# Performance work log

Measured on AMD Instinct MI355X. Metric: run time of the kernel, lower is better.

## Reference

```python
import jax, jax.numpy as jnp
import numpy as np

N_SRC, N_DST, E = 32768, 8192, 65536
NODE_IN, EDGE_IN, HIDDEN = 64, 32, 64


def setup_inputs() -> dict:
    key = jax.random.key(0)
    ks = jax.random.split(key, 8)
    node_features = jax.random.normal(ks[0], (N_SRC, NODE_IN), dtype=jnp.float32)
    edge_features = jax.random.normal(ks[1], (E, EDGE_IN), dtype=jnp.float32)
    src_idx = jax.random.randint(ks[2], (E,), 0, N_SRC, dtype=jnp.int32)
    dst_idx = jax.random.randint(ks[3], (E,), 0, N_DST, dtype=jnp.int32)
    # edge_layer: Linear(edge_in, hidden*node_in); node_layer: Linear(node_in+hidden, hidden)
    s_e = 1.0 / np.sqrt(EDGE_IN)
    s_n = 1.0 / np.sqrt(NODE_IN + HIDDEN)
    W_e = jax.random.uniform(ks[4], (EDGE_IN, HIDDEN * NODE_IN), jnp.float32, -s_e, s_e)
    b_e = jax.random.uniform(ks[5], (HIDDEN * NODE_IN,), jnp.float32, -s_e, s_e)
    W_n = jax.random.uniform(ks[6], (NODE_IN + HIDDEN, HIDDEN), jnp.float32, -s_n, s_n)
    b_n = jax.random.uniform(ks[7], (HIDDEN,), jnp.float32, -s_n, s_n)
    return {"node_features": node_features, "edge_features": edge_features,
            "src_idx": src_idx, "dst_idx": dst_idx,
            "W_e": W_e, "b_e": b_e, "W_n": W_n, "b_n": b_n, "n_dst": N_DST}


def reference(node_features, edge_features, src_idx, dst_idx, W_e, b_e, W_n, b_n, n_dst):
    # Dropout is identity in eval mode.
    # Edge-conditioned weight generation: [E, hidden*node_in] -> [E, hidden, node_in]
    ew = jax.nn.relu(edge_features @ W_e + b_e).reshape(-1, HIDDEN, NODE_IN)
    h_src = node_features[src_idx]                       # [E, node_in] gather
    m = jnp.einsum('ehd,ed->eh', ew, h_src)              # per-edge matvec -> [E, hidden]
    # segment mean over destination nodes (mailbox mean)
    msum = jax.ops.segment_sum(m, dst_idx, num_segments=n_dst)
    cnt = jax.ops.segment_sum(jnp.ones((m.shape[0],), m.dtype), dst_idx, num_segments=n_dst)
    h_neigh = jnp.where(cnt[:, None] > 0, msum / jnp.maximum(cnt[:, None], 1.0), 0.0)
    h_self = node_features[:n_dst]
    h = jnp.concatenate([h_self, h_neigh], axis=1)       # [n_dst, node_in+hidden]
    return jax.nn.relu(h @ W_n + b_n)
```

## Files before the change

kernel.cpp:

```cpp
#include <hip/hip_runtime.h>


typedef float f32x4 __attribute__((ext_vector_type(4)));
typedef __bf16 bf16x8 __attribute__((ext_vector_type(8)));
typedef __bf16 bf16x4 __attribute__((ext_vector_type(4)));

#define E_TOT   65536
#define NDST    8192
#define EPW     72

__global__ void pack_kernel(const float* __restrict__ We, const float* __restrict__ be,
                            __bf16* __restrict__ Wp, float* __restrict__ bp) {
  int tid = blockIdx.x * 256 + threadIdx.x;
  int T = tid >> 6, l = tid & 63;
  int d0 = T >> 2, ht = T & 3;
  int c = l & 15, kg = l >> 4;
  int ncol = (ht * 16 + c) * 64 + d0;
  bf16x8 v;
#pragma unroll
  for (int j = 0; j < 8; ++j) {
    int k = kg * 8 + j;
    v[j] = (__bf16)We[k * 4096 + ncol];
  }
  *reinterpret_cast<bf16x8*>(Wp + tid * 8) = v;
  if (l < 16) bp[T * 16 + l] = be[(ht * 16 + l) * 64 + d0];
}

__global__ __launch_bounds__(256, 4) void edge_kernel(
    const float* __restrict__ nf, const float* __restrict__ ef,
    const int* __restrict__ src, const int* __restrict__ dst,
    const __bf16* __restrict__ Wp, const float* __restrict__ bp,
    float* __restrict__ msum, float* __restrict__ cnt_g) {
  __shared__ __bf16 hs[64 * EPW];
  const int t = threadIdx.x;
  const int eblk = blockIdx.x << 6;

  {
    const int el = t & 63, q = t >> 6;
    const int srow = src[eblk + el];
    const f32x4* nfr = (const f32x4*)(nf + (srow << 6) + (q << 4));
#pragma unroll
    for (int i = 0; i < 4; ++i) {
      f32x4 v = nfr[i];
      const int dbase = (q << 4) + i * 4;
      hs[(dbase + 0) * EPW + el] = (__bf16)v[0];
      hs[(dbase + 1) * EPW + el] = (__bf16)v[1];
      hs[(dbase + 2) * EPW + el] = (__bf16)v[2];
      hs[(dbase + 3) * EPW + el] = (__bf16)v[3];
    }
  }

  const int w = t >> 6;
  const int l = t & 63;
  const int c = l & 15;
  const int g = l >> 4;

  bf16x8 afr[4];
#pragma unroll
  for (int as = 0; as < 4; ++as) {
    const int e = eblk + as * 16 + c;
    const f32x4* p = (const f32x4*)(ef + (e << 5) + (g << 3));
    f32x4 v0 = p[0], v1 = p[1];
    bf16x8 a;
    a[0] = (__bf16)v0[0]; a[1] = (__bf16)v0[1]; a[2] = (__bf16)v0[2]; a[3] = (__bf16)v0[3];
    a[4] = (__bf16)v1[0]; a[5] = (__bf16)v1[1]; a[6] = (__bf16)v1[2]; a[7] = (__bf16)v1[3];
    afr[as] = a;
  }

  __syncthreads();

  f32x4 acc[4];
#pragma unroll
  for (int i = 0; i < 4; ++i) { acc[i][0] = 0.f; acc[i][1] = 0.f; acc[i][2] = 0.f; acc[i][3] = 0.f; }

  const bf16x8* WpV = (const bf16x8*)Wp;
  const f32x4 zero = {0.f, 0.f, 0.f, 0.f};

#pragma unroll 4
  for (int d0 = 0; d0 < 64; ++d0) {
    const int T = d0 * 4 + w;
    const bf16x8 bfr = WpV[T * 64 + l];
    const float bv = bp[T * 16 + c];
    const f32x4 cb = {bv, bv, bv, bv};
#pragma unroll
    for (int as = 0; as < 4; ++as) {
      const bf16x4 hv = *(const bf16x4*)&hs[d0 * EPW + as * 16 + (g << 2)];
      const f32x4 hvf = {(float)hv[0], (float)hv[1], (float)hv[2], (float)hv[3]};
      f32x4 tmp = __builtin_amdgcn_mfma_f32_16x16x32_bf16(afr[as], bfr, cb, 0, 0, 0);
      tmp = __builtin_elementwise_max(tmp, zero);
      acc[as] = tmp * hvf + acc[as];
    }
  }

#pragma unroll
  for (int as = 0; as < 4; ++as) {
#pragma unroll
    for (int r = 0; r < 4; ++r) {
      const int e = eblk + as * 16 + (g << 2) + r;
      const int dd = dst[e];
      unsafeAtomicAdd(msum + (dd << 6) + (w << 4) + c, acc[as][r]);
      if (w == 0 && c == 0) unsafeAtomicAdd(cnt_g + dd, 1.0f);
    }
  }
}

__global__ __launch_bounds__(256) void final_kernel(
    const float* __restrict__ nf, const float* __restrict__ msum,
    const float* __restrict__ cnt, const float* __restrict__ Wn,
    const float* __restrict__ bn, float* __restrict__ out) {
  __shared__ float wn_s[128 * 64];
  const int t = threadIdx.x;
#pragma unroll
  for (int i = 0; i < 8; ++i)
    ((f32x4*)wn_s)[i * 256 + t] = ((const f32x4*)Wn)[i * 256 + t];
  __syncthreads();

  const int w = t >> 6, h = t & 63;
  const int row0 = blockIdx.x * 16 + w * 4;
  const float bv = bn[h];
  float acc[4] = {bv, bv, bv, bv};
  float s[4];
#pragma unroll
  for (int i = 0; i < 4; ++i) {
    const float cv = cnt[row0 + i];
    s[i] = cv > 0.f ? 1.f / cv : 0.f;
  }
#pragma unroll 4
  for (int k = 0; k < 64; ++k) {
    const float wv = wn_s[k * 64 + h];
#pragma unroll
    for (int i = 0; i < 4; ++i)
      acc[i] = fmaf(nf[(row0 + i) * 64 + k], wv, acc[i]);
  }
#pragma unroll 4
  for (int k = 0; k < 64; ++k) {
    const float wv = wn_s[(64 + k) * 64 + h];
#pragma unroll
    for (int i = 0; i < 4; ++i)
      acc[i] = fmaf(msum[(row0 + i) * 64 + k] * s[i], wv, acc[i]);
  }
#pragma unroll
  for (int i = 0; i < 4; ++i)
    out[(row0 + i) * 64 + h] = fmaxf(acc[i], 0.f);
}

extern "C" void kernel_launch(void* const* d_in, const int* in_sizes, int n_in,
                              void* d_out, int out_size, void* d_ws, size_t ws_size,
                              hipStream_t stream) {
  const float* nf  = (const float*)d_in[0];
  const float* ef  = (const float*)d_in[1];
  const int*   src = (const int*)d_in[2];
  const int*   dst = (const int*)d_in[3];
  const float* We  = (const float*)d_in[4];
  const float* be  = (const float*)d_in[5];
  const float* Wn  = (const float*)d_in[6];
  const float* bn  = (const float*)d_in[7];
  float* out = (float*)d_out;

  char* ws = (char*)d_ws;
  float* msum = (float*)ws;
  float* cnt  = (float*)(ws + 2097152);
  const size_t need = 2097152 + 32768 + 262144 + 16384;
  __bf16* Wp;
  float*  bp;
  if (ws_size >= need) {
    Wp = (__bf16*)(ws + 2097152 + 32768);
    bp = (float*)(ws + 2097152 + 32768 + 262144);
  } else {
    Wp = (__bf16*)d_out;
    bp = (float*)((char*)d_out + 262144);
  }

  hipMemsetAsync(msum, 0, 2097152 + 32768, stream);
  pack_kernel<<<64, 256, 0, stream>>>(We, be, Wp, bp);
  edge_kernel<<<E_TOT / 64, 256, 0, stream>>>(nf, ef, src, dst, Wp, bp, msum, cnt);
  final_kernel<<<NDST / 16, 256, 0, stream>>>(nf, msum, cnt, Wn, bn, out);
}
```

Measured before the change: 84.97 us.

## Replace float atomic scatter with CSR sort-by-destination and gather-based segment mean

Adds a counting-sort pipeline (histogram, single-block scan, fill) that builds a CSR list of edges per destination node. The edge kernel now writes per-edge messages densely to a 16 MB buffer instead of issuing atomic adds, and the final kernel gathers and averages each node's messages before the output linear layer. The h_src tile is kept in fp32 in LDS, and the weight fragments are software-prefetched two steps ahead. The aim is to remove atomic contention on msum, at the cost of extra launches, a serial scan, and 16 MB of extra message traffic. This path is only taken when the workspace is large enough.

```diff
diff --git a/kernel.cpp b/kernel.cpp
--- a/kernel.cpp
+++ b/kernel.cpp
@@ -8,6 +8,207 @@
 #define E_TOT   65536
 #define NDST    8192
 #define EPW     72
+#define EPF     68
+
+
+__global__ __launch_bounds__(256) void prep_kernel(
+    const float* __restrict__ We, const float* __restrict__ be,
+    const int* __restrict__ dst, __bf16* __restrict__ Wp, float* __restrict__ bp,
+    int* __restrict__ cnt_i) {
+  const int b = blockIdx.x;
+  if (b < 64) {
+    int tid = b * 256 + threadIdx.x;
+    int T = tid >> 6, l = tid & 63;
+    int d0 = T >> 2, ht = T & 3;
+    int c = l & 15, kg = l >> 4;
+    int ncol = (ht * 16 + c) * 64 + d0;
+    bf16x8 v;
+#pragma unroll
+    for (int j = 0; j < 8; ++j) v[j] = (__bf16)We[(kg * 8 + j) * 4096 + ncol];
+    *reinterpret_cast<bf16x8*>(Wp + tid * 8) = v;
+    if (l < 16) bp[T * 16 + l] = be[(ht * 16 + l) * 64 + d0];
+  } else {
+    int e = (b - 64) * 256 + threadIdx.x;
+    atomicAdd(&cnt_i[dst[e]], 1);
+  }
+}
+
+__global__ __launch_bounds__(256) void scan_kernel(const int* __restrict__ cnt_i,
+                                                   int* __restrict__ off,
+                                                   int* __restrict__ cursor) {
+  __shared__ int part[256];
+  const int t = threadIdx.x;
+  int loc[32];
+  int s = 0;
+#pragma unroll
+  for (int i = 0; i < 32; ++i) { loc[i] = s; s += cnt_i[t * 32 + i]; }
+  part[t] = s;
+  __syncthreads();
+  if (t == 0) {
+    int run = 0;
+#pragma unroll 8
+    for (int j = 0; j < 256; ++j) { int v = part[j]; part[j] = run; run += v; }
+  }
+  __syncthreads();
+  const int base = part[t];
+#pragma unroll
+  for (int i = 0; i < 32; ++i) {
+    int v = base + loc[i];
+    off[t * 32 + i] = v;
+    cursor[t * 32 + i] = v;
+  }
+  if (t == 255) off[8192] = E_TOT;
+}
+
+__global__ void fill_kernel(const int* __restrict__ dst, int* __restrict__ cursor,
+                            int* __restrict__ eid) {
+  int e = blockIdx.x * 256 + threadIdx.x;
+  int slot = atomicAdd(&cursor[dst[e]], 1);
+  eid[slot] = e;
+}
+
+__global__ __launch_bounds__(256, 4) void edge2_kernel(
+    const float* __restrict__ nf, const float* __restrict__ ef,
+    const int* __restrict__ src, const __bf16* __restrict__ Wp,
+    const float* __restrict__ bp, float* __restrict__ m) {
+  __shared__ float hs[64 * EPF];
+  const int t = threadIdx.x;
+  const int eblk = blockIdx.x << 6;
+
+  {
+    const int el = t & 63, q = t >> 6;
+    const int srow = src[eblk + el];
+    const f32x4* nfr = (const f32x4*)(nf + (srow << 6) + (q << 4));
+#pragma unroll
+    for (int i = 0; i < 4; ++i) {
+      f32x4 v = nfr[i];
+      const int dbase = (q << 4) + i * 4;
+      hs[(dbase + 0) * EPF + el] = v[0];
+      hs[(dbase + 1) * EPF + el] = v[1];
+      hs[(dbase + 2) * EPF + el] = v[2];
+      hs[(dbase + 3) * EPF + el] = v[3];
+    }
+  }
+
+  const int w = t >> 6, l = t & 63;
+  const int c = l & 15, g = l >> 4;
+
+  bf16x8 afr[4];
+#pragma unroll
+  for (int as = 0; as < 4; ++as) {
+    const int e = eblk + as * 16 + c;
+    const f32x4* p = (const f32x4*)(ef + (e << 5) + (g << 3));
+    f32x4 v0 = p[0], v1 = p[1];
+    bf16x8 a;
+    a[0] = (__bf16)v0[0]; a[1] = (__bf16)v0[1]; a[2] = (__bf16)v0[2]; a[3] = (__bf16)v0[3];
+    a[4] = (__bf16)v1[0]; a[5] = (__bf16)v1[1]; a[6] = (__bf16)v1[2]; a[7] = (__bf16)v1[3];
+    afr[as] = a;
+  }
+
+  __syncthreads();
+
+  f32x4 acc[4];
+#pragma unroll
+  for (int i = 0; i < 4; ++i) { acc[i][0] = 0.f; acc[i][1] = 0.f; acc[i][2] = 0.f; acc[i][3] = 0.f; }
+
+  const bf16x8* WpV = (const bf16x8*)Wp;
+  const f32x4 zero = {0.f, 0.f, 0.f, 0.f};
+
+  bf16x8 bfrA = WpV[(0 * 4 + w) * 64 + l];
+  float  bvA  = bp[(0 * 4 + w) * 16 + c];
+  bf16x8 bfrB = WpV[(1 * 4 + w) * 64 + l];
+  float  bvB  = bp[(1 * 4 + w) * 16 + c];
+
+  for (int d0 = 0; d0 < 64; d0 += 2) {
+    {
+      const bf16x8 bcur = bfrA;
+      const f32x4 cb = {bvA, bvA, bvA, bvA};
+      if (d0 + 2 < 64) {
+        bfrA = WpV[((d0 + 2) * 4 + w) * 64 + l];
+        bvA  = bp[((d0 + 2) * 4 + w) * 16 + c];
+      }
+#pragma unroll
+      for (int as = 0; as < 4; ++as) {
+        const f32x4 hvf = *(const f32x4*)&hs[d0 * EPF + as * 16 + (g << 2)];
+        f32x4 tmp = __builtin_amdgcn_mfma_f32_16x16x32_bf16(afr[as], bcur, cb, 0, 0, 0);
+        tmp = __builtin_elementwise_max(tmp, zero);
+        acc[as] = tmp * hvf + acc[as];
+      }
+    }
+    {
+      const bf16x8 bcur = bfrB;
+      const f32x4 cb = {bvB, bvB, bvB, bvB};
+      if (d0 + 3 < 64) {
+        bfrB = WpV[((d0 + 3) * 4 + w) * 64 + l];
+        bvB  = bp[((d0 + 3) * 4 + w) * 16 + c];
+      }
+#pragma unroll
+      for (int as = 0; as < 4; ++as) {
+        const f32x4 hvf = *(const f32x4*)&hs[(d0 + 1) * EPF + as * 16 + (g << 2)];
+        f32x4 tmp = __builtin_amdgcn_mfma_f32_16x16x32_bf16(afr[as], bcur, cb, 0, 0, 0);
+        tmp = __builtin_elementwise_max(tmp, zero);
+        acc[as] = tmp * hvf + acc[as];
+      }
+    }
+  }
+
+  const int hbase = (w << 4) + c;
+#pragma unroll
+  for (int as = 0; as < 4; ++as)
+#pragma unroll
+    for (int r = 0; r < 4; ++r) {
+      const int e = eblk + as * 16 + (g << 2) + r;
+      m[(e << 6) + hbase] = acc[as][r];
+    }
+}
+
+__global__ __launch_bounds__(256) void final2_kernel(
+    const float* __restrict__ nf, const float* __restrict__ m,
+    const int* __restrict__ off, const int* __restrict__ eid,
+    const float* __restrict__ Wn, const float* __restrict__ bn,
+    float* __restrict__ out) {
+  __shared__ float wn_s[128 * 64];
+  __shared__ float hn_s[16 * 64];
+  const int t = threadIdx.x;
+#pragma unroll
+  for (int i = 0; i < 8; ++i)
+    ((f32x4*)wn_s)[i * 256 + t] = ((const f32x4*)Wn)[i * 256 + t];
+
+  const int w = t >> 6, h = t & 63;
+  const int row0 = blockIdx.x * 16 + w * 4;
+
+#pragma unroll
+  for (int i = 0; i < 4; ++i) {
+    const int d = row0 + i;
+    const int lo = off[d], hi = off[d + 1];
+    float a = 0.f;
+    for (int j = lo; j < hi; ++j)
+      a += m[(eid[j] << 6) + h];
+    hn_s[(w * 4 + i) * 64 + h] = (hi > lo) ? a * (1.f / (float)(hi - lo)) : 0.f;
+  }
+  __syncthreads();
+
+  const float bv = bn[h];
+  float acc[4] = {bv, bv, bv, bv};
+#pragma unroll 4
+  for (int k = 0; k < 64; ++k) {
+    const float wv = wn_s[k * 64 + h];
+#pragma unroll
+    for (int i = 0; i < 4; ++i)
+      acc[i] = fmaf(nf[(row0 + i) * 64 + k], wv, acc[i]);
+  }
+#pragma unroll 4
+  for (int k = 0; k < 64; ++k) {
+    const float wv = wn_s[(64 + k) * 64 + h];
+#pragma unroll
+    for (int i = 0; i < 4; ++i)
+      acc[i] = fmaf(hn_s[(w * 4 + i) * 64 + k], wv, acc[i]);
+  }
+#pragma unroll
+  for (int i = 0; i < 4; ++i)
+    out[(row0 + i) * 64 + h] = fmaxf(acc[i], 0.f);
+}
+
 
 __global__ void pack_kernel(const float* __restrict__ We, const float* __restrict__ be,
                             __bf16* __restrict__ Wp, float* __restrict__ bp) {
@@ -18,10 +219,7 @@
   int ncol = (ht * 16 + c) * 64 + d0;
   bf16x8 v;
 #pragma unroll
-  for (int j = 0; j < 8; ++j) {
-    int k = kg * 8 + j;
-    v[j] = (__bf16)We[k * 4096 + ncol];
-  }
+  for (int j = 0; j < 8; ++j) v[j] = (__bf16)We[(kg * 8 + j) * 4096 + ncol];
   *reinterpret_cast<bf16x8*>(Wp + tid * 8) = v;
   if (l < 16) bp[T * 16 + l] = be[(ht * 16 + l) * 64 + d0];
 }
@@ -34,7 +232,6 @@
   __shared__ __bf16 hs[64 * EPW];
   const int t = threadIdx.x;
   const int eblk = blockIdx.x << 6;
-
   {
     const int el = t & 63, q = t >> 6;
     const int srow = src[eblk + el];
@@ -49,12 +246,7 @@
       hs[(dbase + 3) * EPW + el] = (__bf16)v[3];
     }
   }
-
-  const int w = t >> 6;
-  const int l = t & 63;
-  const int c = l & 15;
-  const int g = l >> 4;
-
+  const int w = t >> 6, l = t & 63, c = l & 15, g = l >> 4;
   bf16x8 afr[4];
 #pragma unroll
   for (int as = 0; as < 4; ++as) {
@@ -66,16 +258,12 @@
     a[4] = (__bf16)v1[0]; a[5] = (__bf16)v1[1]; a[6] = (__bf16)v1[2]; a[7] = (__bf16)v1[3];
     afr[as] = a;
   }
-
-  __syncthreads();
-
+  __syncthreads();
   f32x4 acc[4];
 #pragma unroll
-  for (int i = 0; i < 4; ++i) { acc[i][0] = 0.f; acc[i][1] = 0.f; acc[i][2] = 0.f; acc[i][3] = 0.f; }
-
+  for (int i = 0; i < 4; ++i) { acc[i][0]=0.f; acc[i][1]=0.f; acc[i][2]=0.f; acc[i][3]=0.f; }
   const bf16x8* WpV = (const bf16x8*)Wp;
   const f32x4 zero = {0.f, 0.f, 0.f, 0.f};
-
 #pragma unroll 4
   for (int d0 = 0; d0 < 64; ++d0) {
     const int T = d0 * 4 + w;
@@ -91,9 +279,8 @@
       acc[as] = tmp * hvf + acc[as];
     }
   }
-
-#pragma unroll
-  for (int as = 0; as < 4; ++as) {
+#pragma unroll
+  for (int as = 0; as < 4; ++as)
 #pragma unroll
     for (int r = 0; r < 4; ++r) {
       const int e = eblk + as * 16 + (g << 2) + r;
@@ -101,7 +288,6 @@
       unsafeAtomicAdd(msum + (dd << 6) + (w << 4) + c, acc[as][r]);
       if (w == 0 && c == 0) unsafeAtomicAdd(cnt_g + dd, 1.0f);
     }
-  }
 }
 
 __global__ __launch_bounds__(256) void final_kernel(
@@ -114,7 +300,6 @@
   for (int i = 0; i < 8; ++i)
     ((f32x4*)wn_s)[i * 256 + t] = ((const f32x4*)Wn)[i * 256 + t];
   __syncthreads();
-
   const int w = t >> 6, h = t & 63;
   const int row0 = blockIdx.x * 16 + w * 4;
   const float bv = bn[h];
@@ -129,20 +314,18 @@
   for (int k = 0; k < 64; ++k) {
     const float wv = wn_s[k * 64 + h];
 #pragma unroll
-    for (int i = 0; i < 4; ++i)
-      acc[i] = fmaf(nf[(row0 + i) * 64 + k], wv, acc[i]);
+    for (int i = 0; i < 4; ++i) acc[i] = fmaf(nf[(row0 + i) * 64 + k], wv, acc[i]);
   }
 #pragma unroll 4
   for (int k = 0; k < 64; ++k) {
     const float wv = wn_s[(64 + k) * 64 + h];
 #pragma unroll
-    for (int i = 0; i < 4; ++i)
-      acc[i] = fmaf(msum[(row0 + i) * 64 + k] * s[i], wv, acc[i]);
-  }
-#pragma unroll
-  for (int i = 0; i < 4; ++i)
-    out[(row0 + i) * 64 + h] = fmaxf(acc[i], 0.f);
-}
+    for (int i = 0; i < 4; ++i) acc[i] = fmaf(msum[(row0 + i) * 64 + k] * s[i], wv, acc[i]);
+  }
+#pragma unroll
+  for (int i = 0; i < 4; ++i) out[(row0 + i) * 64 + h] = fmaxf(acc[i], 0.f);
+}
+
 
 extern "C" void kernel_launch(void* const* d_in, const int* in_sizes, int n_in,
                               void* d_out, int out_size, void* d_ws, size_t ws_size,
@@ -156,23 +339,48 @@
   const float* Wn  = (const float*)d_in[6];
   const float* bn  = (const float*)d_in[7];
   float* out = (float*)d_out;
-
   char* ws = (char*)d_ws;
-  float* msum = (float*)ws;
-  float* cnt  = (float*)(ws + 2097152);
-  const size_t need = 2097152 + 32768 + 262144 + 16384;
-  __bf16* Wp;
-  float*  bp;
-  if (ws_size >= need) {
-    Wp = (__bf16*)(ws + 2097152 + 32768);
-    bp = (float*)(ws + 2097152 + 32768 + 262144);
+
+  const size_t OFF_M      = 0;
+  const size_t OFF_OFF    = 16777216;
+  const size_t OFF_CURSOR = OFF_OFF + 36864;
+  const size_t OFF_CNTI   = OFF_CURSOR + 32768;
+  const size_t OFF_EID    = OFF_CNTI + 32768;
+  const size_t OFF_WP     = OFF_EID + 262144;
+  const size_t OFF_BP     = OFF_WP + 262144;
+  const size_t NEED_FAST  = OFF_BP + 16384;
+
+  if (ws_size >= NEED_FAST) {
+    float*  m      = (float*)(ws + OFF_M);
+    int*    off    = (int*)(ws + OFF_OFF);
+    int*    cursor = (int*)(ws + OFF_CURSOR);
+    int*    cnt_i  = (int*)(ws + OFF_CNTI);
+    int*    eid    = (int*)(ws + OFF_EID);
+    __bf16* Wp     = (__bf16*)(ws + OFF_WP);
+    float*  bp     = (float*)(ws + OFF_BP);
+
+    hipMemsetAsync(cnt_i, 0, 32768, stream);
+    prep_kernel<<<320, 256, 0, stream>>>(We, be, dst, Wp, bp, cnt_i);
+    scan_kernel<<<1, 256, 0, stream>>>(cnt_i, off, cursor);
+    fill_kernel<<<E_TOT / 256, 256, 0, stream>>>(dst, cursor, eid);
+    edge2_kernel<<<E_TOT / 64, 256, 0, stream>>>(nf, ef, src, Wp, bp, m);
+    final2_kernel<<<NDST / 16, 256, 0, stream>>>(nf, m, off, eid, Wn, bn, out);
   } else {
-    Wp = (__bf16*)d_out;
-    bp = (float*)((char*)d_out + 262144);
-  }
-
-  hipMemsetAsync(msum, 0, 2097152 + 32768, stream);
-  pack_kernel<<<64, 256, 0, stream>>>(We, be, Wp, bp);
-  edge_kernel<<<E_TOT / 64, 256, 0, stream>>>(nf, ef, src, dst, Wp, bp, msum, cnt);
-  final_kernel<<<NDST / 16, 256, 0, stream>>>(nf, msum, cnt, Wn, bn, out);
-}
+    float* msum = (float*)ws;
+    float* cnt  = (float*)(ws + 2097152);
+    const size_t need = 2097152 + 32768 + 262144 + 16384;
+    __bf16* Wp;
+    float*  bp;
+    if (ws_size >= need) {
+      Wp = (__bf16*)(ws + 2097152 + 32768);
+      bp = (float*)(ws + 2097152 + 32768 + 262144);
+    } else {
+      Wp = (__bf16*)d_out;
+      bp = (float*)((char*)d_out + 262144);
+    }
+    hipMemsetAsync(msum, 0, 2097152 + 32768, stream);
+    pack_kernel<<<64, 256, 0, stream>>>(We, be, Wp, bp);
+    edge_kernel<<<E_TOT / 64, 256, 0, stream>>>(nf, ef, src, dst, Wp, bp, msum, cnt);
+    final_kernel<<<NDST / 16, 256, 0, stream>>>(nf, msum, cnt, Wn, bn, out);
+  }
+}
```

New measurement: 98.17 us. 15.5% more time.
